# Optimization experiments

Measured on AMD Instinct MI355X. Metric: run time of the kernel, lower is better.

Reference implementation:

```python
import jax, jax.numpy as jnp
import numpy as np

B = 8192
IN = 2048
H = 2048


def setup_inputs() -> dict:
    key = jax.random.key(0)
    ks = jax.random.split(key, 6)
    stdv = 1.0 / np.sqrt(H)
    return {
        "x": jax.random.normal(ks[0], (B, IN), dtype=jnp.float32),
        "h_prev": jax.random.normal(ks[1], (B, H), dtype=jnp.float32),
        "c_prev": jax.random.normal(ks[2], (B, H), dtype=jnp.float32),
        "weight_ih": jax.random.normal(ks[3], (4 * H, IN), dtype=jnp.float32) * stdv,
        "weight_hh": jax.random.normal(ks[4], (4 * H, H), dtype=jnp.float32) * stdv,
        "bias": jax.random.normal(ks[5], (4 * H,), dtype=jnp.float32) * stdv,
    }


def reference(x, h_prev, c_prev, weight_ih, weight_hh, bias):
    # gates: [B, 4H] = x @ W_ih^T + h_prev @ W_hh^T + b
    gates = x @ weight_ih.T + h_prev @ weight_hh.T + bias
    i, f, j, o = jnp.split(gates, 4, axis=1)
    i = jax.nn.sigmoid(i)
    f = jax.nn.sigmoid(f)
    o = jax.nn.sigmoid(o)
    j = jnp.tanh(j)
    # cap_input_gate=True: input gate capped by (1 - f)
    c = f * c_prev + jnp.minimum(1.0 - f, i) * j
    h = o * jnp.tanh(c)
    return (h, c)
```

## Files before the change

kernel.cpp:

```cpp
#include <hip/hip_runtime.h>

#define DEVI __device__ __forceinline__

typedef __attribute__((ext_vector_type(8))) __bf16 bf16x8;
typedef __attribute__((ext_vector_type(4))) float floatx4;

constexpr int Bsz = 8192;
constexpr int Hd  = 2048;
constexpr int INd = 2048;
constexpr int N1  = Bsz * INd;

DEVI unsigned short f2bf_rne(float f) {
  unsigned int u = __float_as_uint(f);
  u += 0x7FFFu + ((u >> 16) & 1u);
  return (unsigned short)(u >> 16);
}

__global__ void cvt4(const float* __restrict__ s0, const float* __restrict__ s1,
                     const float* __restrict__ s2, const float* __restrict__ s3,
                     unsigned short* __restrict__ dst) {
  const float* src = (blockIdx.y == 0) ? s0 : (blockIdx.y == 1) ? s1
                   : (blockIdx.y == 2) ? s2 : s3;
  unsigned short* out = dst + (size_t)blockIdx.y * N1;
  const int nv = N1 / 4;
  for (int i = blockIdx.x * blockDim.x + threadIdx.x; i < nv;
       i += gridDim.x * blockDim.x) {
    float4 v = ((const float4*)src)[i];
    ushort4 o;
    o.x = f2bf_rne(v.x); o.y = f2bf_rne(v.y);
    o.z = f2bf_rne(v.z); o.w = f2bf_rne(v.w);
    ((ushort4*)out)[i] = o;
  }
}

DEVI void gload_lds16(const void* g, void* l) {
  __builtin_amdgcn_global_load_lds(
      (const __attribute__((address_space(1))) void*)g,
      (__attribute__((address_space(3))) void*)l, 16, 0, 0);
}

DEVI float sigm(float x) { return 1.0f / (1.0f + __expf(-x)); }

__global__ __launch_bounds__(512, 2) void lstm_gemm(
    const unsigned short* __restrict__ ws,
    const float* __restrict__ bias,
    const float* __restrict__ c_prev,
    float* __restrict__ out_h,
    float* __restrict__ out_c) {
  __shared__ __align__(16) unsigned short sm[4 * 256 * 64];
  char* smc = (char*)sm;

  const unsigned short* xb  = ws;
  const unsigned short* hb  = ws + (size_t)N1;
  const unsigned short* wih = ws + (size_t)2 * N1;
  const unsigned short* whh = ws + (size_t)3 * N1;

  const int tid  = threadIdx.x;
  const int lane = tid & 63;
  const int wid  = tid >> 6;
  const int wm   = wid >> 2, wn = wid & 3;
  const int lr   = lane & 15, lk = lane >> 4;
  const int lr8  = lane >> 3;
  const int swc  = ((lane & 7) ^ lr8) * 8;

  const int wg = blockIdx.x;
  const int x8 = wg & 7;
  const int lc = wg >> 3;
  const int bc = (x8 & 3) * 8 + (lc & 7);
  const int rb = ((x8 >> 2) * 16 + (lc >> 3)) * 256;

  unsigned int aOff[2][2], bOff[2][2];
#pragma unroll
  for (int h = 0; h < 2; ++h)
#pragma unroll
    for (int j = 0; j < 2; ++j) {
      const int arow = rb + h * 128 + j * 64 + wid * 8 + lr8;
      aOff[h][j] = (unsigned)arow * 2048u + (unsigned)swc;
      const int c  = h * 128 + j * 64 + wid * 8 + lr8;
      const int cf = c >> 4, ce = c & 15;
      const int gate = (cf & 1) | ((cf >> 2) & 2);
      const int hch  = (cf >> 1) & 3;
      const int brow = gate * 2048 + bc * 64 + hch * 16 + ce;
      bOff[h][j] = (unsigned)brow * 2048u + (unsigned)swc;
    }

  floatx4 acc[2][4][2][2];
#pragma unroll
  for (int a = 0; a < 2; ++a)
#pragma unroll
    for (int b = 0; b < 4; ++b)
#pragma unroll
      for (int c = 0; c < 2; ++c)
#pragma unroll
        for (int d = 0; d < 2; ++d)
          acc[a][b][c][d] = (floatx4){0.f, 0.f, 0.f, 0.f};

#define STAGE_A(ts, h) {                                                      \
    const int bs_ = (ts) & 1;                                                 \
    const unsigned short* s_ = (((ts) < 32) ? xb : hb) + (((ts) & 31) * 64);  \
    gload_lds16(s_ + aOff[h][0], smc + bs_ * 32768 + ((h) * 128 + wid * 8) * 128);        \
    gload_lds16(s_ + aOff[h][1], smc + bs_ * 32768 + ((h) * 128 + 64 + wid * 8) * 128); }
#define STAGE_B(ts, h) {                                                      \
    const int bs_ = (ts) & 1;                                                 \
    const unsigned short* s_ = (((ts) < 32) ? wih : whh) + (((ts) & 31) * 64);\
    gload_lds16(s_ + bOff[h][0], smc + 65536 + bs_ * 32768 + ((h) * 128 + wid * 8) * 128);        \
    gload_lds16(s_ + bOff[h][1], smc + 65536 + bs_ * 32768 + ((h) * 128 + 64 + wid * 8) * 128); }

#define LDA(DST, QM)                                                          \
  _Pragma("unroll") for (int mr = 0; mr < 4; ++mr)                            \
    _Pragma("unroll") for (int s = 0; s < 2; ++s) {                           \
      const int row  = (QM) * 128 + wm * 64 + mr * 16 + lr;                   \
      const int phys = (s * 4 + lk) ^ (row & 7);                              \
      DST[mr][s] = *(const bf16x8*)(Ab + row * 128 + phys * 16); }
#define LDB(DST, QN)                                                          \
  _Pragma("unroll") for (int nc = 0; nc < 2; ++nc)                            \
    _Pragma("unroll") for (int s = 0; s < 2; ++s) {                           \
      const int row  = ((QN) * 8 + wn * 2 + nc) * 16 + lr;                    \
      const int phys = (s * 4 + lk) ^ (row & 7);                              \
      DST[nc][s] = *(const bf16x8*)(Bb + row * 128 + phys * 16); }
#define MFMA16(QM, QN, AF, BG)                                                \
  __builtin_amdgcn_s_setprio(1);                                              \
  _Pragma("unroll") for (int mr = 0; mr < 4; ++mr)                            \
    _Pragma("unroll") for (int nc = 0; nc < 2; ++nc)                          \
      _Pragma("unroll") for (int s = 0; s < 2; ++s)                           \
        acc[QM][mr][QN][nc] = __builtin_amdgcn_mfma_f32_16x16x32_bf16(        \
            AF[mr][s], BG[nc][s], acc[QM][mr][QN][nc], 0, 0, 0);              \
  __builtin_amdgcn_s_setprio(0);
#define BAR  asm volatile("s_barrier" ::: "memory")
#define VM4  asm volatile("s_waitcnt vmcnt(4)" ::: "memory")
#define VM0  asm volatile("s_waitcnt vmcnt(0)" ::: "memory")
#define NOP  (void)0

#define KTILE(BETA, S1, S2a, S2b, S3, W4) {                                   \
    const char* Ab = smc + (BETA) * 32768;                                    \
    const char* Bb = smc + 65536 + (BETA) * 32768;                            \
    bf16x8 afA[4][2], afB[4][2], bg0[2][2], bg1[2][2];                        \
    LDA(afA, 0); LDB(bg0, 0); S1;                                             \
    MFMA16(0, 0, afA, bg0); BAR;                                              \
    LDA(afB, 1); S2a; S2b;                                                    \
    MFMA16(1, 0, afB, bg0); BAR;                                              \
    LDB(bg1, 1); S3;                                                          \
    MFMA16(1, 1, afB, bg1); BAR;                                              \
    W4;                                                                       \
    MFMA16(0, 1, afA, bg1); BAR;                                              \
  }

  STAGE_B(0, 0); STAGE_A(0, 1); STAGE_B(0, 1);
  STAGE_A(0, 0); STAGE_B(1, 0); STAGE_A(1, 1);
  VM4;
  BAR;

  for (int t = 0; t < 62; ++t) {
    KTILE(t & 1, STAGE_A(t + 1, 0), STAGE_B(t + 1, 1),
          STAGE_B(t + 2, 0), STAGE_A(t + 2, 1), VM4);
  }
  KTILE(0, STAGE_A(63, 0), STAGE_B(63, 1), NOP, NOP, VM0);
  KTILE(1, NOP, NOP, NOP, NOP, NOP);

  const int hcol = bc * 64 + wn * 16 + lr;
  const float b_i = bias[hcol];
  const float b_f = bias[2048 + hcol];
  const float b_j = bias[4096 + hcol];
  const float b_o = bias[6144 + hcol];
#pragma unroll
  for (int qm = 0; qm < 2; ++qm)
#pragma unroll
    for (int mr = 0; mr < 4; ++mr)
#pragma unroll
      for (int r = 0; r < 4; ++r) {
        const int row = rb + qm * 128 + wm * 64 + mr * 16 + lk * 4 + r;
        const float gi = acc[qm][mr][0][0][r] + b_i;
        const float gf = acc[qm][mr][0][1][r] + b_f;
        const float gj = acc[qm][mr][1][0][r] + b_j;
        const float go = acc[qm][mr][1][1][r] + b_o;
        const float iv = sigm(gi);
        const float fv = sigm(gf);
        const float jv = tanhf(gj);
        const float ov = sigm(go);
        const size_t idx = (size_t)row * 2048 + hcol;
        const float cp = c_prev[idx];
        const float cv = fv * cp + fminf(1.0f - fv, iv) * jv;
        out_h[idx] = ov * tanhf(cv);
        out_c[idx] = cv;
      }
}

extern "C" void kernel_launch(void* const* d_in, const int* in_sizes, int n_in,
                              void* d_out, int out_size, void* d_ws, size_t ws_size,
                              hipStream_t stream) {
  const float* x      = (const float*)d_in[0];
  const float* h_prev = (const float*)d_in[1];
  const float* c_prev = (const float*)d_in[2];
  const float* w_ih   = (const float*)d_in[3];
  const float* w_hh   = (const float*)d_in[4];
  const float* bias   = (const float*)d_in[5];

  float* out_h = (float*)d_out;
  float* out_c = out_h + (size_t)Bsz * Hd;
  unsigned short* wsb = (unsigned short*)d_ws;

  dim3 cgrid(2048, 4);
  cvt4<<<cgrid, 256, 0, stream>>>(x, h_prev, w_ih, w_hh, wsb);

  lstm_gemm<<<1024, 512, 0, stream>>>(wsb, bias, c_prev, out_h, out_c);
}
```

Baseline: 578.4 us.

## Prefetch next k-tile fragments from LDS across tiles in LSTM GEMM

Restructures the k-tile loop so the A quadrant-0 and B quadrant-0 register fragments for the next tile are read from the other LDS buffer at the end of the current tile. The loop is unrolled by two with ping-pong B fragment registers, the vmcnt wait drops from 4 to 2, an extra barrier is added, and the prologue staging order changes. The goal is to hide LDS read latency behind MFMA work across tile boundaries. In exchange it needs more VGPRs, which could hurt occupancy under launch_bounds(512,2), and the altered load ordering risks races on the shared buffers.

```diff
diff --git a/kernel.cpp b/kernel.cpp
--- a/kernel.cpp
+++ b/kernel.cpp
@@ -95,6 +95,8 @@
         for (int d = 0; d < 2; ++d)
           acc[a][b][c][d] = (floatx4){0.f, 0.f, 0.f, 0.f};
 
+  bf16x8 afA0[4][2], afA1[4][2], bgB1[2][2], bgB0a[2][2], bgB0b[2][2];
+
 #define STAGE_A(ts, h) {                                                      \
     const int bs_ = (ts) & 1;                                                 \
     const unsigned short* s_ = (((ts) < 32) ? xb : hb) + (((ts) & 31) * 64);  \
@@ -106,18 +108,18 @@
     gload_lds16(s_ + bOff[h][0], smc + 65536 + bs_ * 32768 + ((h) * 128 + wid * 8) * 128);        \
     gload_lds16(s_ + bOff[h][1], smc + 65536 + bs_ * 32768 + ((h) * 128 + 64 + wid * 8) * 128); }
 
-#define LDA(DST, QM)                                                          \
+#define LDA_Q(DST, QM, BASE)                                                  \
   _Pragma("unroll") for (int mr = 0; mr < 4; ++mr)                            \
     _Pragma("unroll") for (int s = 0; s < 2; ++s) {                           \
       const int row  = (QM) * 128 + wm * 64 + mr * 16 + lr;                   \
       const int phys = (s * 4 + lk) ^ (row & 7);                              \
-      DST[mr][s] = *(const bf16x8*)(Ab + row * 128 + phys * 16); }
-#define LDB(DST, QN)                                                          \
+      DST[mr][s] = *(const bf16x8*)((BASE) + row * 128 + phys * 16); }
+#define LDB_Q(DST, QN, BASE)                                                  \
   _Pragma("unroll") for (int nc = 0; nc < 2; ++nc)                            \
     _Pragma("unroll") for (int s = 0; s < 2; ++s) {                           \
       const int row  = ((QN) * 8 + wn * 2 + nc) * 16 + lr;                    \
       const int phys = (s * 4 + lk) ^ (row & 7);                              \
-      DST[nc][s] = *(const bf16x8*)(Bb + row * 128 + phys * 16); }
+      DST[nc][s] = *(const bf16x8*)((BASE) + row * 128 + phys * 16); }
 #define MFMA16(QM, QN, AF, BG)                                                \
   __builtin_amdgcn_s_setprio(1);                                              \
   _Pragma("unroll") for (int mr = 0; mr < 4; ++mr)                            \
@@ -127,35 +129,49 @@
             AF[mr][s], BG[nc][s], acc[QM][mr][QN][nc], 0, 0, 0);              \
   __builtin_amdgcn_s_setprio(0);
 #define BAR  asm volatile("s_barrier" ::: "memory")
-#define VM4  asm volatile("s_waitcnt vmcnt(4)" ::: "memory")
+#define VM2  asm volatile("s_waitcnt vmcnt(2)" ::: "memory")
 #define VM0  asm volatile("s_waitcnt vmcnt(0)" ::: "memory")
 #define NOP  (void)0
-
-#define KTILE(BETA, S1, S2a, S2b, S3, W4) {                                   \
-    const char* Ab = smc + (BETA) * 32768;                                    \
-    const char* Bb = smc + 65536 + (BETA) * 32768;                            \
-    bf16x8 afA[4][2], afB[4][2], bg0[2][2], bg1[2][2];                        \
-    LDA(afA, 0); LDB(bg0, 0); S1;                                             \
-    MFMA16(0, 0, afA, bg0); BAR;                                              \
-    LDA(afB, 1); S2a; S2b;                                                    \
-    MFMA16(1, 0, afB, bg0); BAR;                                              \
-    LDB(bg1, 1); S3;                                                          \
-    MFMA16(1, 1, afB, bg1); BAR;                                              \
-    W4;                                                                       \
-    MFMA16(0, 1, afA, bg1); BAR;                                              \
-  }
-
-  STAGE_B(0, 0); STAGE_A(0, 1); STAGE_B(0, 1);
-  STAGE_A(0, 0); STAGE_B(1, 0); STAGE_A(1, 1);
-  VM4;
+#define ADVR(B0N) { LDA_Q(afA0, 0, Abn); LDB_Q(B0N, 0, Bbn); }
+
+#define KTILE(T, BETA, B0C, S1, S2a, S2b, S4, VMW, ADV) {                     \
+    const char* Ab  = smc + (BETA) * 32768;                                   \
+    const char* Bb  = smc + 65536 + (BETA) * 32768;                           \
+    const char* Abn = smc + ((BETA) ^ 1) * 32768;                             \
+    const char* Bbn = smc + 65536 + ((BETA) ^ 1) * 32768;                     \
+    (void)Abn; (void)Bbn;                                                     \
+     LDB_Q(bgB1, 1, Bb); S1;                                         \
+    MFMA16(0, 0, afA0, B0C); BAR;                                             \
+     LDA_Q(afA1, 1, Ab); S2a; S2b;                                   \
+    MFMA16(0, 1, afA0, bgB1); BAR;                                            \
+     MFMA16(1, 1, afA1, bgB1); BAR;                                  \
+     VMW; BAR;                                                       \
+    ADV; S4;                                                                  \
+    MFMA16(1, 0, afA1, B0C); BAR;                                             \
+  }
+
+  STAGE_A(0, 0); STAGE_A(0, 1); STAGE_B(0, 0); STAGE_B(0, 1);
+  STAGE_B(1, 0);
+  VM0;
   BAR;
-
-  for (int t = 0; t < 62; ++t) {
-    KTILE(t & 1, STAGE_A(t + 1, 0), STAGE_B(t + 1, 1),
-          STAGE_B(t + 2, 0), STAGE_A(t + 2, 1), VM4);
-  }
-  KTILE(0, STAGE_A(63, 0), STAGE_B(63, 1), NOP, NOP, VM0);
-  KTILE(1, NOP, NOP, NOP, NOP, NOP);
+  {
+    const char* Ab0 = smc;
+    const char* Bb0 = smc + 65536;
+    LDA_Q(afA0, 0, Ab0);
+    LDB_Q(bgB0a, 0, Bb0);
+  }
+  STAGE_A(1, 1);
+
+  for (int u = 0; u < 31; ++u) {
+    const int t0 = 2 * u;
+    KTILE(t0,     0, bgB0a, STAGE_A(t0 + 1, 0), STAGE_B(t0 + 1, 1),
+          STAGE_B(t0 + 2, 0), STAGE_A(t0 + 2, 1), VM2, ADVR(bgB0b));
+    KTILE(t0 + 1, 1, bgB0b, STAGE_A(t0 + 2, 0), STAGE_B(t0 + 2, 1),
+          STAGE_B(t0 + 3, 0), STAGE_A(t0 + 3, 1), VM2, ADVR(bgB0a));
+  }
+  KTILE(62, 0, bgB0a, STAGE_A(63, 0), STAGE_B(63, 1), NOP, NOP, VM0,
+        ADVR(bgB0b));
+  KTILE(63, 1, bgB0b, NOP, NOP, NOP, NOP, NOP, NOP);
 
   const int hcol = bc * 64 + wn * 16 + lr;
   const float b_i = bias[hcol];
```

New measurement: 835.6 us. 44.5% more time.
